# Kernel tuning notes

Hardware: AMD Instinct MI355X
Metric: run time of the kernel (lower is better)

The kernel has to match this reference:

```python
import jax, jax.numpy as jnp
import numpy as np

D = 256       # d_model
NH = 8        # heads
K = 7         # neighborhood kernel size
DFF = 1024    # feedforward dim
EPS = 1e-5
B, H, W = 4, 56, 56


def layer_norm(x, g, b):
    m = jnp.mean(x, axis=-1, keepdims=True)
    v = jnp.mean((x - m) ** 2, axis=-1, keepdims=True)
    return (x - m) * jax.lax.rsqrt(v + EPS) * g + b


def neighborhood_attn(x, W_qkv, b_qkv, W_proj, b_proj):
    # NATTEN NeighborhoodAttention2D: each query attends to a KxK window
    # centered on it, clamped (shifted) at borders so every query sees K*K keys.
    Bx, Hx, Wx, C = x.shape
    hd = C // NH
    qkv = x @ W_qkv + b_qkv                      # [B,H,W,3C]
    q, k, v = jnp.split(qkv, 3, axis=-1)
    q = q.reshape(Bx, Hx, Wx, NH, hd)
    k = k.reshape(Bx, Hx, Wx, NH, hd)
    v = v.reshape(Bx, Hx, Wx, NH, hd)
    # neighbor index grids: start = clip(i - K//2, 0, H-K), window = start + [0..K)
    ih = jnp.clip(jnp.arange(Hx) - K // 2, 0, Hx - K)[:, None] + jnp.arange(K)  # [H,K]
    iw = jnp.clip(jnp.arange(Wx) - K // 2, 0, Wx - K)[:, None] + jnp.arange(K)  # [W,K]
    # gather K/V neighborhoods -> [B,H,W,K,K,NH,hd]
    k_nb = k[:, ih[:, None, :, None], iw[None, :, None, :]]
    v_nb = v[:, ih[:, None, :, None], iw[None, :, None, :]]
    attn = jnp.einsum('bhwnd,bhwijnd->bhwnij', q, k_nb) * (hd ** -0.5)
    attn = jax.nn.softmax(attn.reshape(Bx, Hx, Wx, NH, K * K), axis=-1)
    attn = attn.reshape(Bx, Hx, Wx, NH, K, K)
    out = jnp.einsum('bhwnij,bhwijnd->bhwnd', attn, v_nb).reshape(Bx, Hx, Wx, C)
    return out @ W_proj + b_proj


def setup_inputs() -> dict:
    key = jax.random.key(0)
    ks = jax.random.split(key, 8)
    s = 0.02
    return {
        'x': jax.random.normal(ks[0], (B, H, W, D), dtype=jnp.float32),
        'W_qkv': jax.random.normal(ks[1], (D, 3 * D), dtype=jnp.float32) * s,
        'b_qkv': jnp.zeros((3 * D,), dtype=jnp.float32),
        'W_proj': jax.random.normal(ks[2], (D, D), dtype=jnp.float32) * s,
        'b_proj': jnp.zeros((D,), dtype=jnp.float32),
        'W1': jax.random.normal(ks[3], (D, DFF), dtype=jnp.float32) * s,
        'b1': jnp.zeros((DFF,), dtype=jnp.float32),
        'W2': jax.random.normal(ks[4], (DFF, D), dtype=jnp.float32) * s,
        'b2': jnp.zeros((D,), dtype=jnp.float32),
        'g1': jnp.ones((D,), dtype=jnp.float32),
        'be1': jnp.zeros((D,), dtype=jnp.float32),
        'g2': jnp.ones((D,), dtype=jnp.float32),
        'be2': jnp.zeros((D,), dtype=jnp.float32),
    }


def reference(x, W_qkv, b_qkv, W_proj, b_proj, W1, b1, W2, b2, g1, be1, g2, be2):
    # norm_first=False (post-norm): x = norm1(x + mha(x)); x = norm2(x + ff(x))
    a = neighborhood_attn(x, W_qkv, b_qkv, W_proj, b_proj)
    x = layer_norm(x + a, g1, be1)
    f = jax.nn.relu(x @ W1 + b1) @ W2 + b2
    return layer_norm(x + f, g2, be2)
```

## Files before the change

kernel.cpp:

```cpp
#include <hip/hip_runtime.h>
#include <math.h>

#define BATCH 4
#define HH 56
#define WW 56
#define DMODEL 256
#define NHEADS 8
#define HD 32
#define NNB 49
#define NTOK (BATCH*HH*WW)

#define HALO 22
#define NHTOK (HALO*HALO)
#define KV_PAD 40

typedef __attribute__((ext_vector_type(8))) short s16x8;
typedef __attribute__((ext_vector_type(4))) float f32x4;
typedef __attribute__((ext_vector_type(2))) float f32x2;

__device__ inline unsigned short f2b(float f) {
    union { float f; unsigned int u; } v; v.f = f;
    unsigned int r = v.u + 0x7FFF + ((v.u >> 16) & 1);
    return (unsigned short)(r >> 16);
}
__device__ inline float b2f(unsigned short u) {
    union { float f; unsigned int u; } v; v.u = ((unsigned int)u) << 16;
    return v.f;
}

__device__ __forceinline__ f32x2 unpk(unsigned int u) {
    union { unsigned int u; float f; } lo, hi;
    lo.u = u << 16;
    hi.u = u & 0xffff0000u;
    return f32x2{lo.f, hi.f};
}

__device__ __forceinline__ f32x2 pk_fma(f32x2 a, f32x2 b, f32x2 c) {
#if __has_builtin(__builtin_elementwise_fma)
    return __builtin_elementwise_fma(a, b, c);
#else
    return f32x2{fmaf(a.x, b.x, c.x), fmaf(a.y, b.y, c.y)};
#endif
}

__device__ __forceinline__ void async16(const unsigned short* g, unsigned short* l) {
    __builtin_amdgcn_global_load_lds(
        (const __attribute__((address_space(1))) unsigned int*)g,
        (__attribute__((address_space(3))) unsigned int*)l, 16, 0, 0);
}

#define XCAST_BLOCKS 1568
__global__ __launch_bounds__(256)
void prep_kernel(const float* __restrict__ x,
                 const float* __restrict__ Wq, const float* __restrict__ Wp,
                 const float* __restrict__ W1, const float* __restrict__ W2,
                 unsigned short* __restrict__ xb,
                 unsigned short* __restrict__ Wqb, unsigned short* __restrict__ Wpb,
                 unsigned short* __restrict__ W1b, unsigned short* __restrict__ W2b)
{
    if (blockIdx.x < XCAST_BLOCKS) {
        const int i = blockIdx.x * 256 + threadIdx.x;
        const float4* xp = (const float4*)x + (size_t)i * 2;
        const float4 a = xp[0], b = xp[1];
        s16x8 o;
        o[0] = (short)f2b(a.x); o[1] = (short)f2b(a.y);
        o[2] = (short)f2b(a.z); o[3] = (short)f2b(a.w);
        o[4] = (short)f2b(b.x); o[5] = (short)f2b(b.y);
        o[6] = (short)f2b(b.z); o[7] = (short)f2b(b.w);
        *((s16x8*)xb + i) = o;
        return;
    }
    int i = (blockIdx.x - XCAST_BLOCKS) * 256 + threadIdx.x;
    if (i < 196608) {
        int n = i >> 8, k = i & 255;
        Wqb[i] = f2b(Wq[k * 768 + n]);
    } else if ((i -= 196608) < 65536) {
        int n = i >> 8, k = i & 255;
        Wpb[i] = f2b(Wp[k * 256 + n]);
    } else if ((i -= 65536) < 262144) {
        int n = i >> 8, k = i & 255;
        W1b[i] = f2b(W1[k * 1024 + n]);
    } else {
        i -= 262144;
        int n = i >> 10, k = i & 1023;
        W2b[i] = f2b(W2[k * 256 + n]);
    }
}

template<int BN>
__global__ __launch_bounds__(256)
void gemm_k(const unsigned short* __restrict__ Ab,
            const unsigned short* __restrict__ Bt, const float* __restrict__ bias,
            float* __restrict__ outf, unsigned short* __restrict__ outb,
            int M, int N, int K, int relu)
{
    constexpr int NB  = BN / 32;
    constexpr int BPW = BN / 32;
    __shared__ unsigned short As[2][128 * 64];
    __shared__ unsigned short Bs[2][BN * 64];

    const int tid = threadIdx.x;
    const int bm = blockIdx.y * 128, bn = blockIdx.x * BN;
    const int wid = tid >> 6, lane = tid & 63;
    const int wm = (wid >> 1) * 64, wn = (wid & 1) * (BN / 2);
    const int row16 = lane & 15, quad = lane >> 4;
    const int crow = lane >> 3, ck8 = (lane & 7) * 8;

    f32x4 acc[4][NB] = {};

    auto stage = [&](int buf, int k0) {
        #pragma unroll
        for (int c = 0; c < 4; ++c) {
            const int ch = wid * 4 + c;
            async16(Ab + (size_t)(bm + ch * 8 + crow) * K + k0 + ck8, As[buf] + ch * 512);
        }
        #pragma unroll
        for (int c = 0; c < BPW; ++c) {
            const int ch = wid * BPW + c;
            async16(Bt + (size_t)(bn + ch * 8 + crow) * K + k0 + ck8, Bs[buf] + ch * 512);
        }
    };
    auto compute = [&](int buf) {
        #pragma unroll
        for (int kc = 0; kc < 2; ++kc) {
            s16x8 af[4], bf[NB];
            #pragma unroll
            for (int i = 0; i < 4; ++i)
                af[i] = *(const s16x8*)(As[buf] + (wm + i * 16 + row16) * 64 + kc * 32 + quad * 8);
            #pragma unroll
            for (int j = 0; j < NB; ++j)
                bf[j] = *(const s16x8*)(Bs[buf] + (wn + j * 16 + row16) * 64 + kc * 32 + quad * 8);
            #pragma unroll
            for (int i = 0; i < 4; ++i)
                #pragma unroll
                for (int j = 0; j < NB; ++j)
                    acc[i][j] = __builtin_amdgcn_mfma_f32_16x16x32_bf16(af[i], bf[j], acc[i][j], 0, 0, 0);
        }
    };

    stage(0, 0);
    __syncthreads();
    for (int k0 = 0; k0 < K; k0 += 128) {
        stage(1, k0 + 64);
        compute(0);
        __syncthreads();
        if (k0 + 128 < K) stage(0, k0 + 128);
        compute(1);
        __syncthreads();
    }

    #pragma unroll
    for (int j = 0; j < NB; ++j) {
        const int col = bn + wn + j * 16 + row16;
        const float bb = bias[col];
        #pragma unroll
        for (int i = 0; i < 4; ++i) {
            const int r0 = bm + wm + i * 16 + quad * 4;
            #pragma unroll
            for (int reg = 0; reg < 4; ++reg) {
                float v = acc[i][j][reg] + bb;
                if (relu) v = fmaxf(v, 0.f);
                if (outf) outf[(size_t)(r0 + reg) * N + col] = v;
                if (outb) outb[(size_t)(r0 + reg) * N + col] = f2b(v);
            }
        }
    }
}

__global__ __launch_bounds__(256)
void gemm_ln(const unsigned short* __restrict__ Ab, const unsigned short* __restrict__ Bt,
             const float* __restrict__ bias, const float* __restrict__ resid,
             const float* __restrict__ g, const float* __restrict__ beta,
             float* __restrict__ outf, unsigned short* __restrict__ outb, int K)
{
    __shared__ unsigned short As[2][32 * 64];
    __shared__ unsigned short Bs[2][256 * 64];

    const int tid = threadIdx.x;
    const int bm = blockIdx.x * 32;
    const int wid = tid >> 6, lane = tid & 63;
    const int wn = wid * 64;
    const int row16 = lane & 15, quad = lane >> 4;
    const int crow = lane >> 3, ck8 = (lane & 7) * 8;

    f32x4 acc[2][4] = {};

    auto stage = [&](int buf, int k0) {
        #pragma unroll
        for (int c = 0; c < 9; ++c) {
            const int ch = wid * 9 + c;
            if (ch < 4) {
                async16(Ab + (size_t)(bm + ch * 8 + crow) * K + k0 + ck8, As[buf] + ch * 512);
            } else {
                const int bc = ch - 4;
                async16(Bt + (size_t)(bc * 8 + crow) * K + k0 + ck8, Bs[buf] + bc * 512);
            }
        }
    };
    auto compute = [&](int buf) {
        #pragma unroll
        for (int kc = 0; kc < 2; ++kc) {
            s16x8 af[2], bf[4];
            #pragma unroll
            for (int i = 0; i < 2; ++i)
                af[i] = *(const s16x8*)(As[buf] + (i * 16 + row16) * 64 + kc * 32 + quad * 8);
            #pragma unroll
            for (int j = 0; j < 4; ++j)
                bf[j] = *(const s16x8*)(Bs[buf] + (wn + j * 16 + row16) * 64 + kc * 32 + quad * 8);
            #pragma unroll
            for (int i = 0; i < 2; ++i)
                #pragma unroll
                for (int j = 0; j < 4; ++j)
                    acc[i][j] = __builtin_amdgcn_mfma_f32_16x16x32_bf16(af[i], bf[j], acc[i][j], 0, 0, 0);
        }
    };

    stage(0, 0);
    __syncthreads();
    for (int k0 = 0; k0 < K; k0 += 128) {
        stage(1, k0 + 64);
        compute(0);
        __syncthreads();
        if (k0 + 128 < K) stage(0, k0 + 128);
        compute(1);
        __syncthreads();
    }

    float bb[4], gv[4], bev[4];
    #pragma unroll
    for (int j = 0; j < 4; ++j) {
        const int col = wn + j * 16 + row16;
        bb[j] = bias[col]; gv[j] = g[col]; bev[j] = beta[col];
    }
    #pragma unroll
    for (int i = 0; i < 2; ++i) {
        #pragma unroll
        for (int reg = 0; reg < 4; ++reg) {
            const size_t rb = (size_t)(bm + i * 16 + quad * 4 + reg) * 256;
            #pragma unroll
            for (int j = 0; j < 4; ++j)
                acc[i][j][reg] += bb[j] + resid[rb + wn + j * 16 + row16];
        }
    }

    float* red = (float*)As[0];
    #pragma unroll
    for (int i = 0; i < 2; ++i) {
        #pragma unroll
        for (int reg = 0; reg < 4; ++reg) {
            float s1 = 0.f, s2 = 0.f;
            #pragma unroll
            for (int j = 0; j < 4; ++j) {
                const float t = acc[i][j][reg];
                s1 += t; s2 += t * t;
            }
            #pragma unroll
            for (int o = 1; o < 16; o <<= 1) {
                s1 += __shfl_xor(s1, o, 64);
                s2 += __shfl_xor(s2, o, 64);
            }
            if (row16 == 0) {
                const int lrow = i * 16 + quad * 4 + reg;
                red[lrow * 8 + wid * 2]     = s1;
                red[lrow * 8 + wid * 2 + 1] = s2;
            }
        }
    }
    __syncthreads();
    float* stats = red + 256;
    if (tid < 32) {
        const float S1 = red[tid*8] + red[tid*8+2] + red[tid*8+4] + red[tid*8+6];
        const float S2 = red[tid*8+1] + red[tid*8+3] + red[tid*8+5] + red[tid*8+7];
        const float m = S1 * (1.0f / 256.0f);
        const float var = S2 * (1.0f / 256.0f) - m * m;
        stats[tid * 2]     = m;
        stats[tid * 2 + 1] = rsqrtf(var + 1e-5f);
    }
    __syncthreads();

    #pragma unroll
    for (int i = 0; i < 2; ++i) {
        #pragma unroll
        for (int reg = 0; reg < 4; ++reg) {
            const int lrow = i * 16 + quad * 4 + reg;
            const float m = stats[lrow * 2], r = stats[lrow * 2 + 1];
            const size_t rb = (size_t)(bm + lrow) * 256;
            #pragma unroll
            for (int j = 0; j < 4; ++j) {
                const int col = wn + j * 16 + row16;
                const float o = (acc[i][j][reg] - m) * r * gv[j] + bev[j];
                outf[rb + col] = o;
                if (outb) outb[rb + col] = f2b(o);
            }
        }
    }
}

__global__ __launch_bounds__(256, 2)
void natt_kernel(const unsigned short* __restrict__ qkvb, unsigned short* __restrict__ att)
{
    const int blk  = blockIdx.x;
    const int head = blk & 7;
    const int t2   = blk >> 3;
    const int tile = t2 & 15;
    const int b    = t2 >> 4;
    const int r0 = (tile >> 2) * 16, c0 = (tile & 3) * 16;
    const int hs = min(max(r0 - 3, 0), 34);
    const int ws = min(max(c0 - 3, 0), 34);

    __shared__ unsigned short Ks[NHTOK * KV_PAD];
    __shared__ unsigned short Vs[NHTOK * KV_PAD];

    const int tid = threadIdx.x;

    #pragma unroll
    for (int it = 0; it < 8; ++it) {
        const int t = it * 64 + (tid >> 2);
        if (t < NHTOK) {
            const int hr = t / HALO, hc = t - hr * HALO;
            const size_t rb = ((size_t)((b * 56 + hs + hr) * 56 + (ws + hc))) * 768;
            const int d8 = (tid & 3) * 8;
            *(s16x8*)(Ks + t * KV_PAD + d8) = *(const s16x8*)(qkvb + rb + 256 + head * 32 + d8);
            *(s16x8*)(Vs + t * KV_PAD + d8) = *(const s16x8*)(qkvb + rb + 512 + head * 32 + d8);
        }
    }

    const int qh = min(r0 + (tid >> 4), 55);
    const int qw = min(c0 + (tid & 15), 55);
    const int tok = (b * 56 + qh) * 56 + qw;
    const int ro = min(max(qh - 3, 0), 49) - hs;
    const int co = min(max(qw - 3, 0), 49) - ws;

    f32x2 qf[16];
    {
        const unsigned int* qp = (const unsigned int*)(qkvb + (size_t)tok * 768 + head * 32);
        #pragma unroll
        for (int p = 0; p < 16; ++p)
            qf[p] = unpk(qp[p]) * 0.17677669529663687f;
    }
    __syncthreads();

    f32x2 acc[16] = {};
    float sum = 0.f;
    for (int i = 0; i < 7; ++i) {
        const int trow = (ro + i) * HALO + co;
        #pragma unroll
        for (int j = 0; j < 7; ++j) {
            const unsigned int* kp = (const unsigned int*)(Ks + (trow + j) * KV_PAD);
            const unsigned int* vp = (const unsigned int*)(Vs + (trow + j) * KV_PAD);
            const uint4 ka = *(const uint4*)(kp);
            const uint4 kb = *(const uint4*)(kp + 4);
            const uint4 kc = *(const uint4*)(kp + 8);
            const uint4 kd = *(const uint4*)(kp + 12);
            const uint4 va = *(const uint4*)(vp);
            const uint4 vb = *(const uint4*)(vp + 4);
            const uint4 vc = *(const uint4*)(vp + 8);
            const uint4 vd = *(const uint4*)(vp + 12);
            f32x2 sa = {0.f, 0.f}, sb = {0.f, 0.f};
            sa = pk_fma(qf[0],  unpk(ka.x), sa);  sb = pk_fma(qf[1],  unpk(ka.y), sb);
            sa = pk_fma(qf[2],  unpk(ka.z), sa);  sb = pk_fma(qf[3],  unpk(ka.w), sb);
            sa = pk_fma(qf[4],  unpk(kb.x), sa);  sb = pk_fma(qf[5],  unpk(kb.y), sb);
            sa = pk_fma(qf[6],  unpk(kb.z), sa);  sb = pk_fma(qf[7],  unpk(kb.w), sb);
            sa = pk_fma(qf[8],  unpk(kc.x), sa);  sb = pk_fma(qf[9],  unpk(kc.y), sb);
            sa = pk_fma(qf[10], unpk(kc.z), sa);  sb = pk_fma(qf[11], unpk(kc.w), sb);
            sa = pk_fma(qf[12], unpk(kd.x), sa);  sb = pk_fma(qf[13], unpk(kd.y), sb);
            sa = pk_fma(qf[14], unpk(kd.z), sa);  sb = pk_fma(qf[15], unpk(kd.w), sb);
            const float p = __expf(sa.x + sa.y + sb.x + sb.y);
            sum += p;
            const f32x2 pv = {p, p};
            acc[0]  = pk_fma(pv, unpk(va.x), acc[0]);
            acc[1]  = pk_fma(pv, unpk(va.y), acc[1]);
            acc[2]  = pk_fma(pv, unpk(va.z), acc[2]);
            acc[3]  = pk_fma(pv, unpk(va.w), acc[3]);
            acc[4]  = pk_fma(pv, unpk(vb.x), acc[4]);
            acc[5]  = pk_fma(pv, unpk(vb.y), acc[5]);
            acc[6]  = pk_fma(pv, unpk(vb.z), acc[6]);
            acc[7]  = pk_fma(pv, unpk(vb.w), acc[7]);
            acc[8]  = pk_fma(pv, unpk(vc.x), acc[8]);
            acc[9]  = pk_fma(pv, unpk(vc.y), acc[9]);
            acc[10] = pk_fma(pv, unpk(vc.z), acc[10]);
            acc[11] = pk_fma(pv, unpk(vc.w), acc[11]);
            acc[12] = pk_fma(pv, unpk(vd.x), acc[12]);
            acc[13] = pk_fma(pv, unpk(vd.y), acc[13]);
            acc[14] = pk_fma(pv, unpk(vd.z), acc[14]);
            acc[15] = pk_fma(pv, unpk(vd.w), acc[15]);
        }
    }
    const float inv = 1.0f / sum;

    unsigned short* op = att + (size_t)tok * DMODEL + head * 32;
    #pragma unroll
    for (int d4 = 0; d4 < 8; ++d4) {
        ushort4 o;
        o.x = f2b(acc[d4 * 2].x     * inv);
        o.y = f2b(acc[d4 * 2].y     * inv);
        o.z = f2b(acc[d4 * 2 + 1].x * inv);
        o.w = f2b(acc[d4 * 2 + 1].y * inv);
        *(ushort4*)(op + d4 * 4) = o;
    }
}

extern "C" void kernel_launch(void* const* d_in, const int* in_sizes, int n_in,
                              void* d_out, int out_size, void* d_ws, size_t ws_size,
                              hipStream_t stream)
{
    const float* x      = (const float*)d_in[0];
    const float* W_qkv  = (const float*)d_in[1];
    const float* b_qkv  = (const float*)d_in[2];
    const float* W_proj = (const float*)d_in[3];
    const float* b_proj = (const float*)d_in[4];
    const float* W1     = (const float*)d_in[5];
    const float* b1     = (const float*)d_in[6];
    const float* W2     = (const float*)d_in[7];
    const float* b2     = (const float*)d_in[8];
    const float* g1     = (const float*)d_in[9];
    const float* be1    = (const float*)d_in[10];
    const float* g2     = (const float*)d_in[11];
    const float* be2    = (const float*)d_in[12];
    float* out = (float*)d_out;

    char* ws = (char*)d_ws;
    const int M = NTOK;

    unsigned short* qkvb = (unsigned short*)ws;
    unsigned short* h    = (unsigned short*)ws;
    unsigned short* attb = (unsigned short*)(ws + 38535168);
    float*          xn   = (float*)(ws + 57802752);
    unsigned short* xnb  = (unsigned short*)(ws + 70647808);
    unsigned short* Wqb  = (unsigned short*)(ws + 77070336);
    unsigned short* Wpb  = Wqb + 196608;
    unsigned short* W1b  = Wpb + 65536;
    unsigned short* W2b  = W1b + 262144;
    unsigned short* xb   = (unsigned short*)(ws + 78643200);

    dim3 blk(256);

    prep_kernel<<<dim3(XCAST_BLOCKS + 3072), blk, 0, stream>>>(
        x, W_qkv, W_proj, W1, W2, xb, Wqb, Wpb, W1b, W2b);

    gemm_k<128><<<dim3(6, 98), blk, 0, stream>>>(xb, Wqb, b_qkv, nullptr, qkvb, M, 768, 256, 0);

    natt_kernel<<<dim3(512), blk, 0, stream>>>(qkvb, attb);

    gemm_ln<<<dim3(M / 32), blk, 0, stream>>>(attb, Wpb, b_proj, x, g1, be1, xn, xnb, 256);

    gemm_k<128><<<dim3(8, 98), blk, 0, stream>>>(xnb, W1b, b1, nullptr, h, M, 1024, 256, 1);

    gemm_ln<<<dim3(M / 32), blk, 0, stream>>>(h, W2b, b2, xn, g2, be2, out, nullptr, 1024);
}
```

Before: 199.2 us.

## Tile weight transpose via LDS and double gemm_ln row tile to 64

The weight prep now transposes and casts to bf16 in 64x64 tiles staged through padded LDS. This replaces strided per-element global reads with coalesced float4 reads and ushort4 writes. The fused GEMM+LayerNorm kernel now uses 512-thread blocks covering 64 rows instead of 32, so each B (weight) tile loaded into LDS is reused by twice as many rows. The cost is fewer blocks, more LDS per block and possibly lower occupancy.

```diff
diff --git a/kernel.cpp b/kernel.cpp
--- a/kernel.cpp
+++ b/kernel.cpp
@@ -50,6 +50,34 @@
 }
 
 #define XCAST_BLOCKS 1568
+
+__device__ __forceinline__ void transpose_tile(
+    const float* __restrict__ src, unsigned short* __restrict__ dst,
+    int K, int N, int kt, int nt, int tid, float* lds )
+{
+    const int k0 = kt * 64, n0 = nt * 64;
+    #pragma unroll
+    for (int p = 0; p < 4; ++p) {
+        const int r  = p * 16 + (tid >> 4);
+        const int c4 = (tid & 15) * 4;
+        const float4 v = *(const float4*)(src + (size_t)(k0 + r) * N + n0 + c4);
+        lds[r * 65 + c4 + 0] = v.x; lds[r * 65 + c4 + 1] = v.y;
+        lds[r * 65 + c4 + 2] = v.z; lds[r * 65 + c4 + 3] = v.w;
+    }
+    __syncthreads();
+    #pragma unroll
+    for (int p = 0; p < 4; ++p) {
+        const int c  = p * 16 + (tid >> 4);
+        const int k4 = (tid & 15) * 4;
+        ushort4 o;
+        o.x = f2b(lds[(k4 + 0) * 65 + c]);
+        o.y = f2b(lds[(k4 + 1) * 65 + c]);
+        o.z = f2b(lds[(k4 + 2) * 65 + c]);
+        o.w = f2b(lds[(k4 + 3) * 65 + c]);
+        *(ushort4*)(dst + (size_t)(n0 + c) * K + k0 + k4) = o;
+    }
+}
+
 __global__ __launch_bounds__(256)
 void prep_kernel(const float* __restrict__ x,
                  const float* __restrict__ Wq, const float* __restrict__ Wp,
@@ -58,8 +86,10 @@
                  unsigned short* __restrict__ Wqb, unsigned short* __restrict__ Wpb,
                  unsigned short* __restrict__ W1b, unsigned short* __restrict__ W2b)
 {
+    __shared__ float lds[64 * 65];
+    const int tid = threadIdx.x;
     if (blockIdx.x < XCAST_BLOCKS) {
-        const int i = blockIdx.x * 256 + threadIdx.x;
+        const int i = blockIdx.x * 256 + tid;
         const float4* xp = (const float4*)x + (size_t)i * 2;
         const float4 a = xp[0], b = xp[1];
         s16x8 o;
@@ -70,20 +100,16 @@
         *((s16x8*)xb + i) = o;
         return;
     }
-    int i = (blockIdx.x - XCAST_BLOCKS) * 256 + threadIdx.x;
-    if (i < 196608) {
-        int n = i >> 8, k = i & 255;
-        Wqb[i] = f2b(Wq[k * 768 + n]);
-    } else if ((i -= 196608) < 65536) {
-        int n = i >> 8, k = i & 255;
-        Wpb[i] = f2b(Wp[k * 256 + n]);
-    } else if ((i -= 65536) < 262144) {
-        int n = i >> 8, k = i & 255;
-        W1b[i] = f2b(W1[k * 1024 + n]);
+    int wb = blockIdx.x - XCAST_BLOCKS;
+    if (wb < 48) {
+        transpose_tile(Wq, Wqb, 256, 768, wb & 3, wb >> 2, tid, lds);
+    } else if ((wb -= 48) < 16) {
+        transpose_tile(Wp, Wpb, 256, 256, wb & 3, wb >> 2, tid, lds);
+    } else if ((wb -= 16) < 64) {
+        transpose_tile(W1, W1b, 256, 1024, wb & 3, wb >> 2, tid, lds);
     } else {
-        i -= 262144;
-        int n = i >> 10, k = i & 1023;
-        W2b[i] = f2b(W2[k * 256 + n]);
+        wb -= 64;
+        transpose_tile(W2, W2b, 1024, 256, wb & 15, wb >> 4, tid, lds);
     }
 }
 
@@ -167,19 +193,20 @@
     }
 }
 
-__global__ __launch_bounds__(256)
+__global__ __launch_bounds__(512)
 void gemm_ln(const unsigned short* __restrict__ Ab, const unsigned short* __restrict__ Bt,
              const float* __restrict__ bias, const float* __restrict__ resid,
              const float* __restrict__ g, const float* __restrict__ beta,
              float* __restrict__ outf, unsigned short* __restrict__ outb, int K)
 {
-    __shared__ unsigned short As[2][32 * 64];
+    __shared__ unsigned short As[2][64 * 64];
     __shared__ unsigned short Bs[2][256 * 64];
 
     const int tid = threadIdx.x;
-    const int bm = blockIdx.x * 32;
+    const int bm = blockIdx.x * 64;
     const int wid = tid >> 6, lane = tid & 63;
-    const int wn = wid * 64;
+    const int wm = (wid >> 2) * 32, wn = (wid & 3) * 64;
+    const int wc = wid & 3;
     const int row16 = lane & 15, quad = lane >> 4;
     const int crow = lane >> 3, ck8 = (lane & 7) * 8;
 
@@ -187,12 +214,12 @@
 
     auto stage = [&](int buf, int k0) {
         #pragma unroll
-        for (int c = 0; c < 9; ++c) {
-            const int ch = wid * 9 + c;
-            if (ch < 4) {
+        for (int c = 0; c < 5; ++c) {
+            const int ch = wid * 5 + c;
+            if (ch < 8) {
                 async16(Ab + (size_t)(bm + ch * 8 + crow) * K + k0 + ck8, As[buf] + ch * 512);
             } else {
-                const int bc = ch - 4;
+                const int bc = ch - 8;
                 async16(Bt + (size_t)(bc * 8 + crow) * K + k0 + ck8, Bs[buf] + bc * 512);
             }
         }
@@ -203,7 +230,7 @@
             s16x8 af[2], bf[4];
             #pragma unroll
             for (int i = 0; i < 2; ++i)
-                af[i] = *(const s16x8*)(As[buf] + (i * 16 + row16) * 64 + kc * 32 + quad * 8);
+                af[i] = *(const s16x8*)(As[buf] + (wm + i * 16 + row16) * 64 + kc * 32 + quad * 8);
             #pragma unroll
             for (int j = 0; j < 4; ++j)
                 bf[j] = *(const s16x8*)(Bs[buf] + (wn + j * 16 + row16) * 64 + kc * 32 + quad * 8);
@@ -236,7 +263,7 @@
     for (int i = 0; i < 2; ++i) {
         #pragma unroll
         for (int reg = 0; reg < 4; ++reg) {
-            const size_t rb = (size_t)(bm + i * 16 + quad * 4 + reg) * 256;
+            const size_t rb = (size_t)(bm + wm + i * 16 + quad * 4 + reg) * 256;
             #pragma unroll
             for (int j = 0; j < 4; ++j)
                 acc[i][j][reg] += bb[j] + resid[rb + wn + j * 16 + row16];
@@ -260,15 +287,15 @@
                 s2 += __shfl_xor(s2, o, 64);
             }
             if (row16 == 0) {
-                const int lrow = i * 16 + quad * 4 + reg;
-                red[lrow * 8 + wid * 2]     = s1;
-                red[lrow * 8 + wid * 2 + 1] = s2;
-            }
-        }
-    }
-    __syncthreads();
-    float* stats = red + 256;
-    if (tid < 32) {
+                const int lrow = wm + i * 16 + quad * 4 + reg;
+                red[lrow * 8 + wc * 2]     = s1;
+                red[lrow * 8 + wc * 2 + 1] = s2;
+            }
+        }
+    }
+    __syncthreads();
+    float* stats = red + 512;
+    if (tid < 64) {
         const float S1 = red[tid*8] + red[tid*8+2] + red[tid*8+4] + red[tid*8+6];
         const float S2 = red[tid*8+1] + red[tid*8+3] + red[tid*8+5] + red[tid*8+7];
         const float m = S1 * (1.0f / 256.0f);
@@ -282,7 +309,7 @@
     for (int i = 0; i < 2; ++i) {
         #pragma unroll
         for (int reg = 0; reg < 4; ++reg) {
-            const int lrow = i * 16 + quad * 4 + reg;
+            const int lrow = wm + i * 16 + quad * 4 + reg;
             const float m = stats[lrow * 2], r = stats[lrow * 2 + 1];
             const size_t rb = (size_t)(bm + lrow) * 256;
             #pragma unroll
@@ -435,16 +462,16 @@
 
     dim3 blk(256);
 
-    prep_kernel<<<dim3(XCAST_BLOCKS + 3072), blk, 0, stream>>>(
+    prep_kernel<<<dim3(XCAST_BLOCKS + 48 + 16 + 64 + 64), blk, 0, stream>>>(
         x, W_qkv, W_proj, W1, W2, xb, Wqb, Wpb, W1b, W2b);
 
     gemm_k<128><<<dim3(6, 98), blk, 0, stream>>>(xb, Wqb, b_qkv, nullptr, qkvb, M, 768, 256, 0);
 
     natt_kernel<<<dim3(512), blk, 0, stream>>>(qkvb, attb);
 
-    gemm_ln<<<dim3(M / 32), blk, 0, stream>>>(attb, Wpb, b_proj, x, g1, be1, xn, xnb, 256);
+    gemm_ln<<<dim3(M / 64), dim3(512), 0, stream>>>(attb, Wpb, b_proj, x, g1, be1, xn, xnb, 256);
 
     gemm_k<128><<<dim3(8, 98), blk, 0, stream>>>(xnb, W1b, b1, nullptr, h, M, 1024, 256, 1);
 
-    gemm_ln<<<dim3(M / 32), blk, 0, stream>>>(h, W2b, b2, xn, g2, be2, out, nullptr, 1024);
-}
+    gemm_ln<<<dim3(M / 64), dim3(512), 0, stream>>>(h, W2b, b2, xn, g2, be2, out, nullptr, 1024);
+}
```

Result: faster. 194.8 us (-2.2%).
